# Kernel optimization log

Hardware: AMD Instinct MI355X
Metric: run time of the kernel (lower is better)

## Reference

```python
import jax, jax.numpy as jnp
import numpy as np

B, N, D_IN, D_OUT = 8, 256, 128, 128
EPS = 1e-5


def setup_inputs() -> dict:
    key = jax.random.key(0)
    ks = jax.random.split(key, 12)
    node_feats = jax.random.normal(ks[0], (B, N, D_IN), dtype=jnp.float32)
    adj_mask = jax.random.randint(ks[1], (B, N, N), 0, 2, dtype=jnp.int32)
    # ensure no fully-masked row (self-loop), matching typical adjacency
    adj_mask = adj_mask.at[:, jnp.arange(N), jnp.arange(N)].set(1)
    rel_positions = jax.random.normal(ks[2], (B, N, N, 2), dtype=jnp.float32)
    s_in = 1.0 / np.sqrt(D_IN)
    s_e = 1.0 / np.sqrt(2 * D_IN + 3)
    s_out = 1.0 / np.sqrt(D_OUT)
    return {
        "node_feats": node_feats,
        "adj_mask": adj_mask,
        "rel_positions": rel_positions,
        "Wn": jax.random.uniform(ks[3], (D_IN, D_OUT), jnp.float32, -s_in, s_in),
        "bn": jax.random.uniform(ks[4], (D_OUT,), jnp.float32, -s_in, s_in),
        "We1": jax.random.uniform(ks[5], (2 * D_IN + 3, D_OUT), jnp.float32, -s_e, s_e),
        "be1": jax.random.uniform(ks[6], (D_OUT,), jnp.float32, -s_e, s_e),
        "We2": jax.random.uniform(ks[7], (D_OUT, 1), jnp.float32, -s_out, s_out),
        "be2": jax.random.uniform(ks[8], (1,), jnp.float32, -s_out, s_out),
        "Wa": jax.random.uniform(ks[9], (D_OUT, D_OUT), jnp.float32, -s_out, s_out),
        "ba": jax.random.uniform(ks[10], (D_OUT,), jnp.float32, -s_out, s_out),
        "gamma": jnp.ones((D_OUT,), jnp.float32),
        "beta": jnp.zeros((D_OUT,), jnp.float32),
    }


def reference(node_feats, adj_mask, rel_positions, Wn, bn, We1, be1, We2, be2, Wa, ba, gamma, beta):
    D = node_feats.shape[-1]
    h = node_feats @ Wn + bn                                # (B,N,Dout)
    # Edge MLP first layer, factored to avoid the (B,N,N,2D+3) concat:
    # edge_input = [h_i, h_j, rel, dist]; Linear(edge_input) splits by rows of We1.
    a_i = node_feats @ We1[:D]                              # source-node part  (B,N,Dout)
    a_j = node_feats @ We1[D:2 * D]                         # target-node part  (B,N,Dout)
    rel_dist = jnp.linalg.norm(rel_positions, axis=-1, keepdims=True)  # (B,N,N,1)
    rel_feat = jnp.concatenate([rel_positions, rel_dist], axis=-1)     # (B,N,N,3)
    a_rel = rel_feat @ We1[2 * D:]                          # (B,N,N,Dout)
    hidden = jax.nn.relu(a_i[:, :, None, :] + a_j[:, None, :, :] + a_rel + be1)
    edge_scores = (hidden @ We2 + be2)[..., 0]              # (B,N,N)
    edge_scores = jnp.where(adj_mask == 0, -jnp.inf, edge_scores)
    w = jax.nn.softmax(edge_scores, axis=-1)
    w = jnp.where(jnp.isnan(w), 0.0, w)                     # fully-masked rows -> 0
    messages = jnp.einsum("bij,bjd->bid", w, h)             # (B,N,Dout)
    aggregated = jax.nn.relu(messages @ Wa + ba)            # dropout in eval mode -> identity
    x = node_feats + aggregated                             # D_IN == D_OUT -> residual
    mu = jnp.mean(x, axis=-1, keepdims=True)
    var = jnp.mean((x - mu) ** 2, axis=-1, keepdims=True)
    return (x - mu) / jnp.sqrt(var + EPS) * gamma + beta
```

## Files before the change

### kernel.cpp

```cpp
#include <hip/hip_runtime.h>
#include <math.h>

#define BB 8
#define NN 256
#define DD 128

typedef _Float16 h2 __attribute__((ext_vector_type(2)));
union U4 { uint4 u; float4 f; h2 h[8]; };

static __device__ __forceinline__ h2 relu2(h2 v) {
    h2 z = {(_Float16)0, (_Float16)0};
#if __has_builtin(__builtin_elementwise_max)
    return __builtin_elementwise_max(v, z);
#else
    v.x = v.x > z.x ? v.x : z.x;
    v.y = v.y > z.y ? v.y : z.y;
    return v;
#endif
}

static __device__ __forceinline__ float dot2acc(h2 a, h2 b, float c) {
#if __has_builtin(__builtin_amdgcn_fdot2)
    return __builtin_amdgcn_fdot2(a, b, c, false);
#else
    return fmaf((float)a.x, (float)b.x, fmaf((float)a.y, (float)b.y, c));
#endif
}

#define PR 4
__global__ __launch_bounds__(256) void prep_kernel(
    const float* __restrict__ node, const float* __restrict__ Wn,
    const float* __restrict__ bn, const float* __restrict__ We1,
    const float* __restrict__ be1, const float* __restrict__ We2,
    float* __restrict__ h, _Float16* __restrict__ tih,
    _Float16* __restrict__ ajh, _Float16* __restrict__ wth)
{
    __shared__ __align__(16) float sx[PR * DD];
    __shared__ float s_acc[12 * 128];
    int tid = threadIdx.x;
    int cp = tid & 63;
    int rp = (tid >> 6) & 1;
    int ks = tid >> 7;
    int row0 = blockIdx.x * PR;
    if (tid < 128) {
        int rr = tid >> 5, cc = (tid & 31) << 2;
        *(float4*)&sx[rr * DD + cc] = *(const float4*)&node[(size_t)(row0 + rr) * DD + cc];
    }
    if (blockIdx.x == 0 && tid < 128) {
        wth[0 * 128 + tid] = (_Float16)We1[(size_t)(2 * DD + 0) * DD + tid];
        wth[1 * 128 + tid] = (_Float16)We1[(size_t)(2 * DD + 1) * DD + tid];
        wth[2 * 128 + tid] = (_Float16)We1[(size_t)(2 * DD + 2) * DD + tid];
        wth[3 * 128 + tid] = (_Float16)We2[tid];
    }
    __syncthreads();
    int d0 = cp << 1;
    int ra = rp << 1, rb = ra | 1;
    float ah[2] = {0.f, 0.f}, ai[2] = {0.f, 0.f}, ajc[2] = {0.f, 0.f};
    float bh[2] = {0.f, 0.f}, bi[2] = {0.f, 0.f}, bjc[2] = {0.f, 0.f};
    int k0 = ks << 6;
    for (int k = k0; k < k0 + 64; k += 4) {
        float4 xa = *(const float4*)&sx[ra * DD + k];
        float4 xb = *(const float4*)&sx[rb * DD + k];
        #pragma unroll
        for (int kk = 0; kk < 4; ++kk) {
            float2 w0 = *(const float2*)&Wn [(size_t)(k + kk) * DD + d0];
            float2 w1 = *(const float2*)&We1[(size_t)(k + kk) * DD + d0];
            float2 w2 = *(const float2*)&We1[(size_t)(DD + k + kk) * DD + d0];
            float xav = (kk == 0) ? xa.x : (kk == 1) ? xa.y : (kk == 2) ? xa.z : xa.w;
            float xbv = (kk == 0) ? xb.x : (kk == 1) ? xb.y : (kk == 2) ? xb.z : xb.w;
            ah[0] = fmaf(xav, w0.x, ah[0]); ah[1] = fmaf(xav, w0.y, ah[1]);
            ai[0] = fmaf(xav, w1.x, ai[0]); ai[1] = fmaf(xav, w1.y, ai[1]);
            ajc[0] = fmaf(xav, w2.x, ajc[0]); ajc[1] = fmaf(xav, w2.y, ajc[1]);
            bh[0] = fmaf(xbv, w0.x, bh[0]); bh[1] = fmaf(xbv, w0.y, bh[1]);
            bi[0] = fmaf(xbv, w1.x, bi[0]); bi[1] = fmaf(xbv, w1.y, bi[1]);
            bjc[0] = fmaf(xbv, w2.x, bjc[0]); bjc[1] = fmaf(xbv, w2.y, bjc[1]);
        }
    }
    int p = (rp << 6) | cp;
    if (ks == 1) {
        s_acc[0 * 128 + p] = ah[0];  s_acc[1 * 128 + p] = ah[1];
        s_acc[2 * 128 + p] = ai[0];  s_acc[3 * 128 + p] = ai[1];
        s_acc[4 * 128 + p] = ajc[0]; s_acc[5 * 128 + p] = ajc[1];
        s_acc[6 * 128 + p] = bh[0];  s_acc[7 * 128 + p] = bh[1];
        s_acc[8 * 128 + p] = bi[0];  s_acc[9 * 128 + p] = bi[1];
        s_acc[10 * 128 + p] = bjc[0]; s_acc[11 * 128 + p] = bjc[1];
    }
    __syncthreads();
    if (ks == 0) {
        float2 bn2  = *(const float2*)&bn[d0];
        float2 be12 = *(const float2*)&be1[d0];
        ah[0] += s_acc[0 * 128 + p] + bn2.x;  ah[1] += s_acc[1 * 128 + p] + bn2.y;
        ai[0] += s_acc[2 * 128 + p] + be12.x; ai[1] += s_acc[3 * 128 + p] + be12.y;
        ajc[0] += s_acc[4 * 128 + p];         ajc[1] += s_acc[5 * 128 + p];
        bh[0] += s_acc[6 * 128 + p] + bn2.x;  bh[1] += s_acc[7 * 128 + p] + bn2.y;
        bi[0] += s_acc[8 * 128 + p] + be12.x; bi[1] += s_acc[9 * 128 + p] + be12.y;
        bjc[0] += s_acc[10 * 128 + p];        bjc[1] += s_acc[11 * 128 + p];
        size_t oa = (size_t)(row0 + ra) * DD + d0;
        size_t ob = (size_t)(row0 + rb) * DD + d0;
        *(float2*)&h[oa] = make_float2(ah[0], ah[1]);
        *(float2*)&h[ob] = make_float2(bh[0], bh[1]);
        *(h2*)&tih[oa] = (h2){(_Float16)ai[0], (_Float16)ai[1]};
        *(h2*)&tih[ob] = (h2){(_Float16)bi[0], (_Float16)bi[1]};
        *(h2*)&ajh[oa] = (h2){(_Float16)ajc[0], (_Float16)ajc[1]};
        *(h2*)&ajh[ob] = (h2){(_Float16)bjc[0], (_Float16)bjc[1]};
    }
}

#define IT 4
__global__ __launch_bounds__(256, 2) void edge_kernel(
    const _Float16* __restrict__ tih, const _Float16* __restrict__ ajh,
    const _Float16* __restrict__ wth, const float* __restrict__ rel,
    const int* __restrict__ adj, const float* __restrict__ be2,
    const float* __restrict__ h, const float* __restrict__ Wa,
    const float* __restrict__ ba, const float* __restrict__ node,
    const float* __restrict__ gamma, const float* __restrict__ beta,
    float* __restrict__ out)
{
    __shared__ __align__(16) float s_buf[NN * 32];
    __shared__ __align__(16) float s_w[NN * 4];
    __shared__ __align__(16) float s_m[DD * 4];
    __shared__ float s_red[IT][4];
    __shared__ float s_red2[IT][2][2];

    int tid = threadIdx.x;
    int b  = blockIdx.x >> 6;
    int i0 = (blockIdx.x & 63) << 2;
    int j = tid;

    const float2* rel2 = (const float2*)rel;
    float sc[IT];
    int msk[IT];
    h2 rxh[IT], ryh[IT], dsh[IT];
    float be2v = be2[0];
    #pragma unroll
    for (int r = 0; r < IT; ++r) {
        float2 rp = rel2[(size_t)(b * NN + i0 + r) * NN + j];
        float ds = sqrtf(rp.x * rp.x + rp.y * rp.y);
        _Float16 xh = (_Float16)rp.x, yh = (_Float16)rp.y, dh = (_Float16)ds;
        rxh[r] = (h2){xh, xh}; ryh[r] = (h2){yh, yh}; dsh[r] = (h2){dh, dh};
        msk[r] = adj[(size_t)(b * NN + i0 + r) * NN + j];
        sc[r] = be2v;
    }
    const _Float16* TIH = tih + (size_t)(b * NN + i0) * DD;
    const _Float16* AJH = ajh + (size_t)b * NN * DD;

    for (int dc = 0; dc < DD; dc += 64) {
        __syncthreads();
        #pragma unroll
        for (int it = 0; it < 8; ++it) {
            int idx = tid + it * 256;
            int rr = idx >> 3, g = idx & 7;
            float4 v = *(const float4*)&AJH[(size_t)rr * DD + dc + (g << 3)];
            *(float4*)&s_buf[rr * 32 + ((g ^ (rr & 7)) << 2)] = v;
        }
        __syncthreads();
        #pragma unroll
        for (int gg = 0; gg < 8; ++gg) {
            U4 a; a.f = *(const float4*)&s_buf[j * 32 + ((gg ^ (j & 7)) << 2)];
            int dd = dc + (gg << 3);
            U4 w0u, w1u, w2u, e2u;
            w0u.u = *(const uint4*)&wth[0 * 128 + dd];
            w1u.u = *(const uint4*)&wth[1 * 128 + dd];
            w2u.u = *(const uint4*)&wth[2 * 128 + dd];
            e2u.u = *(const uint4*)&wth[3 * 128 + dd];
            #pragma unroll
            for (int r = 0; r < IT; ++r) {
                U4 t; t.u = *(const uint4*)&TIH[r * DD + dd];
                #pragma unroll
                for (int u = 0; u < 4; ++u) {
                    h2 v = t.h[u] + a.h[u];
                    v = rxh[r] * w0u.h[u] + v;
                    v = ryh[r] * w1u.h[u] + v;
                    v = dsh[r] * w2u.h[u] + v;
                    v = relu2(v);
                    sc[r] = dot2acc(v, e2u.h[u], sc[r]);
                }
            }
        }
    }
    #pragma unroll
    for (int r = 0; r < IT; ++r) if (msk[r] == 0) sc[r] = -3.0e38f;

    int wave = tid >> 6, lane = tid & 63;
    float e[IT];
    {
        float m[IT];
        #pragma unroll
        for (int r = 0; r < IT; ++r) m[r] = sc[r];
        for (int off = 32; off > 0; off >>= 1) {
            #pragma unroll
            for (int r = 0; r < IT; ++r) m[r] = fmaxf(m[r], __shfl_xor(m[r], off));
        }
        if (lane == 0) {
            #pragma unroll
            for (int r = 0; r < IT; ++r) s_red[r][wave] = m[r];
        }
    }
    __syncthreads();
    #pragma unroll
    for (int r = 0; r < IT; ++r) {
        float M = fmaxf(fmaxf(s_red[r][0], s_red[r][1]), fmaxf(s_red[r][2], s_red[r][3]));
        e[r] = (msk[r] == 0) ? 0.f : __expf(sc[r] - M);
    }
    __syncthreads();
    {
        float s[IT];
        #pragma unroll
        for (int r = 0; r < IT; ++r) s[r] = e[r];
        for (int off = 32; off > 0; off >>= 1) {
            #pragma unroll
            for (int r = 0; r < IT; ++r) s[r] += __shfl_xor(s[r], off);
        }
        if (lane == 0) {
            #pragma unroll
            for (int r = 0; r < IT; ++r) s_red[r][wave] = s[r];
        }
    }
    __syncthreads();
    {
        float4 wq;
        float S0 = s_red[0][0] + s_red[0][1] + s_red[0][2] + s_red[0][3];
        float S1 = s_red[1][0] + s_red[1][1] + s_red[1][2] + s_red[1][3];
        float S2 = s_red[2][0] + s_red[2][1] + s_red[2][2] + s_red[2][3];
        float S3 = s_red[3][0] + s_red[3][1] + s_red[3][2] + s_red[3][3];
        wq.x = e[0] * __builtin_amdgcn_rcpf(S0);
        wq.y = e[1] * __builtin_amdgcn_rcpf(S1);
        wq.z = e[2] * __builtin_amdgcn_rcpf(S2);
        wq.w = e[3] * __builtin_amdgcn_rcpf(S3);
        *(float4*)&s_w[j << 2] = wq;
    }
    __syncthreads();

    float* s_part = s_buf;
    int g3 = tid & 31, sl = tid >> 5;
    {
        const float* hb = h + (size_t)b * NN * DD;
        float4 acc[IT];
        #pragma unroll
        for (int r = 0; r < IT; ++r) acc[r] = make_float4(0.f, 0.f, 0.f, 0.f);
        for (int q = 0; q < 32; ++q) {
            int jj = (sl << 5) + q;
            float4 hv = *(const float4*)&hb[(size_t)jj * DD + (g3 << 2)];
            float4 wv = *(const float4*)&s_w[jj << 2];
            acc[0].x = fmaf(wv.x, hv.x, acc[0].x); acc[0].y = fmaf(wv.x, hv.y, acc[0].y);
            acc[0].z = fmaf(wv.x, hv.z, acc[0].z); acc[0].w = fmaf(wv.x, hv.w, acc[0].w);
            acc[1].x = fmaf(wv.y, hv.x, acc[1].x); acc[1].y = fmaf(wv.y, hv.y, acc[1].y);
            acc[1].z = fmaf(wv.y, hv.z, acc[1].z); acc[1].w = fmaf(wv.y, hv.w, acc[1].w);
            acc[2].x = fmaf(wv.z, hv.x, acc[2].x); acc[2].y = fmaf(wv.z, hv.y, acc[2].y);
            acc[2].z = fmaf(wv.z, hv.z, acc[2].z); acc[2].w = fmaf(wv.z, hv.w, acc[2].w);
            acc[3].x = fmaf(wv.w, hv.x, acc[3].x); acc[3].y = fmaf(wv.w, hv.y, acc[3].y);
            acc[3].z = fmaf(wv.w, hv.z, acc[3].z); acc[3].w = fmaf(wv.w, hv.w, acc[3].w);
        }
        int base = ((sl << 5) + g3) * 20;
        #pragma unroll
        for (int r = 0; r < IT; ++r) *(float4*)&s_part[base + (r << 2)] = acc[r];
    }
    __syncthreads();
    #pragma unroll
    for (int p = 0; p < 2; ++p) {
        int o = tid + (p << 8);
        int r = o >> 7, d = o & 127;
        float s = 0.f;
        #pragma unroll
        for (int s2 = 0; s2 < 8; ++s2)
            s += s_part[((s2 << 5) + (d >> 2)) * 20 + (r << 2) + (d & 3)];
        s_m[(d << 2) + r] = s;
    }
    __syncthreads();

    {
        float4 ac[IT];
        #pragma unroll
        for (int r = 0; r < IT; ++r) ac[r] = make_float4(0.f, 0.f, 0.f, 0.f);
        for (int q = 0; q < 16; ++q) {
            int k = (sl << 4) + q;
            float4 wa = *(const float4*)&Wa[(size_t)k * DD + (g3 << 2)];
            float4 mv = *(const float4*)&s_m[k << 2];
            ac[0].x = fmaf(mv.x, wa.x, ac[0].x); ac[0].y = fmaf(mv.x, wa.y, ac[0].y);
            ac[0].z = fmaf(mv.x, wa.z, ac[0].z); ac[0].w = fmaf(mv.x, wa.w, ac[0].w);
            ac[1].x = fmaf(mv.y, wa.x, ac[1].x); ac[1].y = fmaf(mv.y, wa.y, ac[1].y);
            ac[1].z = fmaf(mv.y, wa.z, ac[1].z); ac[1].w = fmaf(mv.y, wa.w, ac[1].w);
            ac[2].x = fmaf(mv.z, wa.x, ac[2].x); ac[2].y = fmaf(mv.z, wa.y, ac[2].y);
            ac[2].z = fmaf(mv.z, wa.z, ac[2].z); ac[2].w = fmaf(mv.z, wa.w, ac[2].w);
            ac[3].x = fmaf(mv.w, wa.x, ac[3].x); ac[3].y = fmaf(mv.w, wa.y, ac[3].y);
            ac[3].z = fmaf(mv.w, wa.z, ac[3].z); ac[3].w = fmaf(mv.w, wa.w, ac[3].w);
        }
        __syncthreads();
        int base = ((sl << 5) + g3) * 20;
        #pragma unroll
        for (int r = 0; r < IT; ++r) *(float4*)&s_part[base + (r << 2)] = ac[r];
    }
    __syncthreads();

    {
        int d = tid & 127;
        int wh = (tid >> 6) & 1;
        float bad = ba[d], gam = gamma[d], bet = beta[d];
        float xv[2];
        #pragma unroll
        for (int p = 0; p < 2; ++p) {
            int o = tid + (p << 8);
            int r = o >> 7;
            float agg = 0.f;
            #pragma unroll
            for (int s2 = 0; s2 < 8; ++s2)
                agg += s_part[((s2 << 5) + (d >> 2)) * 20 + (r << 2) + (d & 3)];
            float x = node[(size_t)(b * NN + i0 + r) * DD + d] + fmaxf(agg + bad, 0.f);
            xv[p] = x;
            float s1 = x, s2v = x * x;
            for (int off = 32; off > 0; off >>= 1) {
                s1 += __shfl_xor(s1, off);
                s2v += __shfl_xor(s2v, off);
            }
            if (lane == 0) { s_red2[r][wh][0] = s1; s_red2[r][wh][1] = s2v; }
        }
        __syncthreads();
        #pragma unroll
        for (int p = 0; p < 2; ++p) {
            int o = tid + (p << 8);
            int r = o >> 7;
            float t1 = s_red2[r][0][0] + s_red2[r][1][0];
            float t2 = s_red2[r][0][1] + s_red2[r][1][1];
            float mu  = t1 * (1.0f / DD);
            float var = t2 * (1.0f / DD) - mu * mu;
            float inv = rsqrtf(var + 1e-5f);
            out[(size_t)(b * NN + i0 + r) * DD + d] = (xv[p] - mu) * inv * gam + bet;
        }
    }
}

extern "C" void kernel_launch(void* const* d_in, const int* in_sizes, int n_in,
                              void* d_out, int out_size, void* d_ws, size_t ws_size,
                              hipStream_t stream) {
    const float* node = (const float*)d_in[0];
    const int*   adj  = (const int*)d_in[1];
    const float* rel  = (const float*)d_in[2];
    const float* Wn   = (const float*)d_in[3];
    const float* bn   = (const float*)d_in[4];
    const float* We1  = (const float*)d_in[5];
    const float* be1  = (const float*)d_in[6];
    const float* We2  = (const float*)d_in[7];
    const float* be2  = (const float*)d_in[8];
    const float* Wa   = (const float*)d_in[9];
    const float* ba   = (const float*)d_in[10];
    const float* gamma = (const float*)d_in[11];
    const float* beta  = (const float*)d_in[12];
    float* out = (float*)d_out;

    float* ws  = (float*)d_ws;
    const int ROWS = BB * NN * DD;
    float* h        = ws;
    _Float16* tih   = (_Float16*)(ws + ROWS);
    _Float16* ajh   = tih + ROWS;
    _Float16* wth   = ajh + ROWS;

    prep_kernel<<<BB * NN / PR, 256, 0, stream>>>(node, Wn, bn, We1, be1, We2,
                                                  h, tih, ajh, wth);
    edge_kernel<<<BB * NN / IT, 256, 0, stream>>>(tih, ajh, wth, rel, adj, be2,
                                                  h, Wa, ba, node, gamma, beta, out);
}
```

Before: 111.8 us.

## Process eight target rows per 512-thread block and stage full aj tile once

The edge kernel now handles 8 query rows per block with 512 threads, two half-blocks of 4 rows each sharing one shared-memory copy of the aj features. The full 128-wide aj tile is loaded once with a 16-way XOR swizzle instead of two 64-wide chunks, which removes a synchronisation round. The aggregation and Wa projection phases are widened to 8 rows so each h and Wa load is reused across more rows. In exchange shared memory grows to about 72KB of s_buf per block and register pressure rises, which may lower occupancy.

```diff
diff --git a/kernel.cpp b/kernel.cpp
--- a/kernel.cpp
+++ b/kernel.cpp
@@ -106,8 +106,8 @@
     }
 }
 
-#define IT 4
-__global__ __launch_bounds__(256, 2) void edge_kernel(
+#define IT 8
+__global__ __launch_bounds__(512, 2) void edge_kernel(
     const _Float16* __restrict__ tih, const _Float16* __restrict__ ajh,
     const _Float16* __restrict__ wth, const float* __restrict__ rel,
     const int* __restrict__ adj, const float* __restrict__ be2,
@@ -116,118 +116,119 @@
     const float* __restrict__ gamma, const float* __restrict__ beta,
     float* __restrict__ out)
 {
-    __shared__ __align__(16) float s_buf[NN * 32];
-    __shared__ __align__(16) float s_w[NN * 4];
-    __shared__ __align__(16) float s_m[DD * 4];
-    __shared__ float s_red[IT][4];
+    __shared__ __align__(16) float s_buf[18432];
+    __shared__ __align__(16) float s_w[NN * 8];
+    __shared__ __align__(16) float s_m[DD * 8];
+    __shared__ float s_redM[IT][4];
+    __shared__ float s_redS[IT][4];
     __shared__ float s_red2[IT][2][2];
 
     int tid = threadIdx.x;
-    int b  = blockIdx.x >> 6;
-    int i0 = (blockIdx.x & 63) << 2;
-    int j = tid;
+    int b  = blockIdx.x >> 5;
+    int i0 = (blockIdx.x & 31) << 3;
+    int j    = tid & 255;
+    int half = tid >> 8;
+    int rb   = half << 2;
 
     const float2* rel2 = (const float2*)rel;
-    float sc[IT];
-    int msk[IT];
-    h2 rxh[IT], ryh[IT], dsh[IT];
+    float sc[4];
+    int msk[4];
+    h2 rxh[4], ryh[4], dsh[4];
     float be2v = be2[0];
     #pragma unroll
-    for (int r = 0; r < IT; ++r) {
-        float2 rp = rel2[(size_t)(b * NN + i0 + r) * NN + j];
+    for (int r = 0; r < 4; ++r) {
+        float2 rp = rel2[(size_t)(b * NN + i0 + rb + r) * NN + j];
         float ds = sqrtf(rp.x * rp.x + rp.y * rp.y);
         _Float16 xh = (_Float16)rp.x, yh = (_Float16)rp.y, dh = (_Float16)ds;
         rxh[r] = (h2){xh, xh}; ryh[r] = (h2){yh, yh}; dsh[r] = (h2){dh, dh};
-        msk[r] = adj[(size_t)(b * NN + i0 + r) * NN + j];
+        msk[r] = adj[(size_t)(b * NN + i0 + rb + r) * NN + j];
         sc[r] = be2v;
     }
-    const _Float16* TIH = tih + (size_t)(b * NN + i0) * DD;
-    const _Float16* AJH = ajh + (size_t)b * NN * DD;
-
-    for (int dc = 0; dc < DD; dc += 64) {
-        __syncthreads();
+
+    {
+        const _Float16* AJH = ajh + (size_t)b * NN * DD;
         #pragma unroll
         for (int it = 0; it < 8; ++it) {
-            int idx = tid + it * 256;
-            int rr = idx >> 3, g = idx & 7;
-            float4 v = *(const float4*)&AJH[(size_t)rr * DD + dc + (g << 3)];
-            *(float4*)&s_buf[rr * 32 + ((g ^ (rr & 7)) << 2)] = v;
-        }
-        __syncthreads();
-        #pragma unroll
-        for (int gg = 0; gg < 8; ++gg) {
-            U4 a; a.f = *(const float4*)&s_buf[j * 32 + ((gg ^ (j & 7)) << 2)];
-            int dd = dc + (gg << 3);
-            U4 w0u, w1u, w2u, e2u;
-            w0u.u = *(const uint4*)&wth[0 * 128 + dd];
-            w1u.u = *(const uint4*)&wth[1 * 128 + dd];
-            w2u.u = *(const uint4*)&wth[2 * 128 + dd];
-            e2u.u = *(const uint4*)&wth[3 * 128 + dd];
-            #pragma unroll
-            for (int r = 0; r < IT; ++r) {
-                U4 t; t.u = *(const uint4*)&TIH[r * DD + dd];
-                #pragma unroll
-                for (int u = 0; u < 4; ++u) {
-                    h2 v = t.h[u] + a.h[u];
-                    v = rxh[r] * w0u.h[u] + v;
-                    v = ryh[r] * w1u.h[u] + v;
-                    v = dsh[r] * w2u.h[u] + v;
-                    v = relu2(v);
-                    sc[r] = dot2acc(v, e2u.h[u], sc[r]);
-                }
+            int idx = tid + (it << 9);
+            int rr = idx >> 4, g = idx & 15;
+            float4 v = *(const float4*)&AJH[(size_t)rr * DD + (g << 3)];
+            *(float4*)&s_buf[rr * 64 + ((g ^ (rr & 15)) << 2)] = v;
+        }
+    }
+    int tibase = __builtin_amdgcn_readfirstlane((b * NN + i0 + rb) * DD);
+    const _Float16* TIH = tih + tibase;
+    __syncthreads();
+
+    #pragma unroll 4
+    for (int gg = 0; gg < 16; ++gg) {
+        U4 a; a.f = *(const float4*)&s_buf[j * 64 + ((gg ^ (j & 15)) << 2)];
+        int dd = gg << 3;
+        U4 w0u, w1u, w2u, e2u;
+        w0u.u = *(const uint4*)&wth[0 * 128 + dd];
+        w1u.u = *(const uint4*)&wth[1 * 128 + dd];
+        w2u.u = *(const uint4*)&wth[2 * 128 + dd];
+        e2u.u = *(const uint4*)&wth[3 * 128 + dd];
+        #pragma unroll
+        for (int r = 0; r < 4; ++r) {
+            U4 t; t.u = *(const uint4*)&TIH[r * DD + dd];
+            #pragma unroll
+            for (int u = 0; u < 4; ++u) {
+                h2 v = t.h[u] + a.h[u];
+                v = rxh[r] * w0u.h[u] + v;
+                v = ryh[r] * w1u.h[u] + v;
+                v = dsh[r] * w2u.h[u] + v;
+                v = relu2(v);
+                sc[r] = dot2acc(v, e2u.h[u], sc[r]);
             }
         }
     }
     #pragma unroll
-    for (int r = 0; r < IT; ++r) if (msk[r] == 0) sc[r] = -3.0e38f;
-
-    int wave = tid >> 6, lane = tid & 63;
-    float e[IT];
-    {
-        float m[IT];
-        #pragma unroll
-        for (int r = 0; r < IT; ++r) m[r] = sc[r];
+    for (int r = 0; r < 4; ++r) if (msk[r] == 0) sc[r] = -3.0e38f;
+
+    int wave = tid >> 6, wig = wave & 3, lane = tid & 63;
+    float e[4];
+    {
+        float m[4];
+        #pragma unroll
+        for (int r = 0; r < 4; ++r) m[r] = sc[r];
         for (int off = 32; off > 0; off >>= 1) {
             #pragma unroll
-            for (int r = 0; r < IT; ++r) m[r] = fmaxf(m[r], __shfl_xor(m[r], off));
+            for (int r = 0; r < 4; ++r) m[r] = fmaxf(m[r], __shfl_xor(m[r], off));
         }
         if (lane == 0) {
             #pragma unroll
-            for (int r = 0; r < IT; ++r) s_red[r][wave] = m[r];
-        }
-    }
-    __syncthreads();
-    #pragma unroll
-    for (int r = 0; r < IT; ++r) {
-        float M = fmaxf(fmaxf(s_red[r][0], s_red[r][1]), fmaxf(s_red[r][2], s_red[r][3]));
-        e[r] = (msk[r] == 0) ? 0.f : __expf(sc[r] - M);
-    }
-    __syncthreads();
-    {
-        float s[IT];
-        #pragma unroll
-        for (int r = 0; r < IT; ++r) s[r] = e[r];
+            for (int r = 0; r < 4; ++r) s_redM[rb + r][wig] = m[r];
+        }
+    }
+    __syncthreads();
+    {
+        float s[4];
+        #pragma unroll
+        for (int r = 0; r < 4; ++r) {
+            float M = fmaxf(fmaxf(s_redM[rb + r][0], s_redM[rb + r][1]),
+                            fmaxf(s_redM[rb + r][2], s_redM[rb + r][3]));
+            e[r] = (msk[r] == 0) ? 0.f : __expf(sc[r] - M);
+            s[r] = e[r];
+        }
         for (int off = 32; off > 0; off >>= 1) {
             #pragma unroll
-            for (int r = 0; r < IT; ++r) s[r] += __shfl_xor(s[r], off);
+            for (int r = 0; r < 4; ++r) s[r] += __shfl_xor(s[r], off);
         }
         if (lane == 0) {
             #pragma unroll
-            for (int r = 0; r < IT; ++r) s_red[r][wave] = s[r];
+            for (int r = 0; r < 4; ++r) s_redS[rb + r][wig] = s[r];
         }
     }
     __syncthreads();
     {
         float4 wq;
-        float S0 = s_red[0][0] + s_red[0][1] + s_red[0][2] + s_red[0][3];
-        float S1 = s_red[1][0] + s_red[1][1] + s_red[1][2] + s_red[1][3];
-        float S2 = s_red[2][0] + s_red[2][1] + s_red[2][2] + s_red[2][3];
-        float S3 = s_red[3][0] + s_red[3][1] + s_red[3][2] + s_red[3][3];
-        wq.x = e[0] * __builtin_amdgcn_rcpf(S0);
-        wq.y = e[1] * __builtin_amdgcn_rcpf(S1);
-        wq.z = e[2] * __builtin_amdgcn_rcpf(S2);
-        wq.w = e[3] * __builtin_amdgcn_rcpf(S3);
-        *(float4*)&s_w[j << 2] = wq;
+        #pragma unroll
+        for (int r = 0; r < 4; ++r) {
+            float S = s_redS[rb + r][0] + s_redS[rb + r][1] + s_redS[rb + r][2] + s_redS[rb + r][3];
+            float wv = e[r] * __builtin_amdgcn_rcpf(S);
+            ((float*)&wq)[r] = wv;
+        }
+        *(float4*)&s_w[(j << 3) + rb] = wq;
     }
     __syncthreads();
 
@@ -235,76 +236,85 @@
     int g3 = tid & 31, sl = tid >> 5;
     {
         const float* hb = h + (size_t)b * NN * DD;
-        float4 acc[IT];
-        #pragma unroll
-        for (int r = 0; r < IT; ++r) acc[r] = make_float4(0.f, 0.f, 0.f, 0.f);
-        for (int q = 0; q < 32; ++q) {
-            int jj = (sl << 5) + q;
+        float4 acc[8];
+        #pragma unroll
+        for (int r = 0; r < 8; ++r) acc[r] = make_float4(0.f, 0.f, 0.f, 0.f);
+        for (int q = 0; q < 16; ++q) {
+            int jj = (sl << 4) + q;
             float4 hv = *(const float4*)&hb[(size_t)jj * DD + (g3 << 2)];
-            float4 wv = *(const float4*)&s_w[jj << 2];
-            acc[0].x = fmaf(wv.x, hv.x, acc[0].x); acc[0].y = fmaf(wv.x, hv.y, acc[0].y);
-            acc[0].z = fmaf(wv.x, hv.z, acc[0].z); acc[0].w = fmaf(wv.x, hv.w, acc[0].w);
-            acc[1].x = fmaf(wv.y, hv.x, acc[1].x); acc[1].y = fmaf(wv.y, hv.y, acc[1].y);
-            acc[1].z = fmaf(wv.y, hv.z, acc[1].z); acc[1].w = fmaf(wv.y, hv.w, acc[1].w);
-            acc[2].x = fmaf(wv.z, hv.x, acc[2].x); acc[2].y = fmaf(wv.z, hv.y, acc[2].y);
-            acc[2].z = fmaf(wv.z, hv.z, acc[2].z); acc[2].w = fmaf(wv.z, hv.w, acc[2].w);
-            acc[3].x = fmaf(wv.w, hv.x, acc[3].x); acc[3].y = fmaf(wv.w, hv.y, acc[3].y);
-            acc[3].z = fmaf(wv.w, hv.z, acc[3].z); acc[3].w = fmaf(wv.w, hv.w, acc[3].w);
-        }
-        int base = ((sl << 5) + g3) * 20;
-        #pragma unroll
-        for (int r = 0; r < IT; ++r) *(float4*)&s_part[base + (r << 2)] = acc[r];
+            float4 wa = *(const float4*)&s_w[(jj << 3) + 0];
+            float4 wb = *(const float4*)&s_w[(jj << 3) + 4];
+            #pragma unroll
+            for (int r = 0; r < 4; ++r) {
+                float wv = ((float*)&wa)[r];
+                acc[r].x = fmaf(wv, hv.x, acc[r].x); acc[r].y = fmaf(wv, hv.y, acc[r].y);
+                acc[r].z = fmaf(wv, hv.z, acc[r].z); acc[r].w = fmaf(wv, hv.w, acc[r].w);
+            }
+            #pragma unroll
+            for (int r = 0; r < 4; ++r) {
+                float wv = ((float*)&wb)[r];
+                acc[4 + r].x = fmaf(wv, hv.x, acc[4 + r].x); acc[4 + r].y = fmaf(wv, hv.y, acc[4 + r].y);
+                acc[4 + r].z = fmaf(wv, hv.z, acc[4 + r].z); acc[4 + r].w = fmaf(wv, hv.w, acc[4 + r].w);
+            }
+        }
+        int base = ((sl << 5) + g3) * 36;
+        #pragma unroll
+        for (int r = 0; r < 8; ++r) *(float4*)&s_part[base + (r << 2)] = acc[r];
     }
     __syncthreads();
     #pragma unroll
     for (int p = 0; p < 2; ++p) {
-        int o = tid + (p << 8);
+        int o = tid + (p << 9);
         int r = o >> 7, d = o & 127;
         float s = 0.f;
         #pragma unroll
-        for (int s2 = 0; s2 < 8; ++s2)
-            s += s_part[((s2 << 5) + (d >> 2)) * 20 + (r << 2) + (d & 3)];
-        s_m[(d << 2) + r] = s;
-    }
-    __syncthreads();
-
-    {
-        float4 ac[IT];
-        #pragma unroll
-        for (int r = 0; r < IT; ++r) ac[r] = make_float4(0.f, 0.f, 0.f, 0.f);
-        for (int q = 0; q < 16; ++q) {
-            int k = (sl << 4) + q;
-            float4 wa = *(const float4*)&Wa[(size_t)k * DD + (g3 << 2)];
-            float4 mv = *(const float4*)&s_m[k << 2];
-            ac[0].x = fmaf(mv.x, wa.x, ac[0].x); ac[0].y = fmaf(mv.x, wa.y, ac[0].y);
-            ac[0].z = fmaf(mv.x, wa.z, ac[0].z); ac[0].w = fmaf(mv.x, wa.w, ac[0].w);
-            ac[1].x = fmaf(mv.y, wa.x, ac[1].x); ac[1].y = fmaf(mv.y, wa.y, ac[1].y);
-            ac[1].z = fmaf(mv.y, wa.z, ac[1].z); ac[1].w = fmaf(mv.y, wa.w, ac[1].w);
-            ac[2].x = fmaf(mv.z, wa.x, ac[2].x); ac[2].y = fmaf(mv.z, wa.y, ac[2].y);
-            ac[2].z = fmaf(mv.z, wa.z, ac[2].z); ac[2].w = fmaf(mv.z, wa.w, ac[2].w);
-            ac[3].x = fmaf(mv.w, wa.x, ac[3].x); ac[3].y = fmaf(mv.w, wa.y, ac[3].y);
-            ac[3].z = fmaf(mv.w, wa.z, ac[3].z); ac[3].w = fmaf(mv.w, wa.w, ac[3].w);
-        }
-        __syncthreads();
-        int base = ((sl << 5) + g3) * 20;
-        #pragma unroll
-        for (int r = 0; r < IT; ++r) *(float4*)&s_part[base + (r << 2)] = ac[r];
-    }
-    __syncthreads();
-
-    {
-        int d = tid & 127;
-        int wh = (tid >> 6) & 1;
-        float bad = ba[d], gam = gamma[d], bet = beta[d];
+        for (int s2 = 0; s2 < 16; ++s2)
+            s += s_part[((s2 << 5) + (d >> 2)) * 36 + (r << 2) + (d & 3)];
+        s_m[(d << 3) + r] = s;
+    }
+    __syncthreads();
+
+    {
+        float4 ac[8];
+        #pragma unroll
+        for (int r = 0; r < 8; ++r) ac[r] = make_float4(0.f, 0.f, 0.f, 0.f);
+        for (int q = 0; q < 8; ++q) {
+            int k = (sl << 3) + q;
+            float4 wv = *(const float4*)&Wa[(size_t)k * DD + (g3 << 2)];
+            float4 ma = *(const float4*)&s_m[(k << 3) + 0];
+            float4 mb = *(const float4*)&s_m[(k << 3) + 4];
+            #pragma unroll
+            for (int r = 0; r < 4; ++r) {
+                float mv = ((float*)&ma)[r];
+                ac[r].x = fmaf(mv, wv.x, ac[r].x); ac[r].y = fmaf(mv, wv.y, ac[r].y);
+                ac[r].z = fmaf(mv, wv.z, ac[r].z); ac[r].w = fmaf(mv, wv.w, ac[r].w);
+            }
+            #pragma unroll
+            for (int r = 0; r < 4; ++r) {
+                float mv = ((float*)&mb)[r];
+                ac[4 + r].x = fmaf(mv, wv.x, ac[4 + r].x); ac[4 + r].y = fmaf(mv, wv.y, ac[4 + r].y);
+                ac[4 + r].z = fmaf(mv, wv.z, ac[4 + r].z); ac[4 + r].w = fmaf(mv, wv.w, ac[4 + r].w);
+            }
+        }
+        int base = ((sl << 5) + g3) * 36;
+        #pragma unroll
+        for (int r = 0; r < 8; ++r) *(float4*)&s_part[base + (r << 2)] = ac[r];
+    }
+    __syncthreads();
+
+    {
+        int wh = wave & 1;
         float xv[2];
+        int dref = tid & 127;
+        float bad = ba[dref], gam = gamma[dref], bet = beta[dref];
         #pragma unroll
         for (int p = 0; p < 2; ++p) {
-            int o = tid + (p << 8);
-            int r = o >> 7;
+            int o = tid + (p << 9);
+            int r = o >> 7, d = o & 127;
             float agg = 0.f;
             #pragma unroll
-            for (int s2 = 0; s2 < 8; ++s2)
-                agg += s_part[((s2 << 5) + (d >> 2)) * 20 + (r << 2) + (d & 3)];
+            for (int s2 = 0; s2 < 16; ++s2)
+                agg += s_part[((s2 << 5) + (d >> 2)) * 36 + (r << 2) + (d & 3)];
             float x = node[(size_t)(b * NN + i0 + r) * DD + d] + fmaxf(agg + bad, 0.f);
             xv[p] = x;
             float s1 = x, s2v = x * x;
@@ -317,8 +327,8 @@
         __syncthreads();
         #pragma unroll
         for (int p = 0; p < 2; ++p) {
-            int o = tid + (p << 8);
-            int r = o >> 7;
+            int o = tid + (p << 9);
+            int r = o >> 7, d = o & 127;
             float t1 = s_red2[r][0][0] + s_red2[r][1][0];
             float t2 = s_red2[r][0][1] + s_red2[r][1][1];
             float mu  = t1 * (1.0f / DD);
@@ -356,6 +366,6 @@
 
     prep_kernel<<<BB * NN / PR, 256, 0, stream>>>(node, Wn, bn, We1, be1, We2,
                                                   h, tih, ajh, wth);
-    edge_kernel<<<BB * NN / IT, 256, 0, stream>>>(tih, ajh, wth, rel, adj, be2,
+    edge_kernel<<<BB * NN / IT, 512, 0, stream>>>(tih, ajh, wth, rel, adj, be2,
                                                   h, Wa, ba, node, gamma, beta, out);
 }
```

Result: no change. 110.5 us (-1.1%).
